# Performance work log

Measured on AMD Instinct MI355X. Metric: run time of the kernel, lower is better.

Reference implementation:

```python
import jax, jax.numpy as jnp
import numpy as np

B, S, E, H = 2, 2048, 1024, 16
DH = E // H
SCALE = DH ** -0.5


def setup_inputs() -> dict:
    key = jax.random.key(0)
    ks = jax.random.split(key, 11)
    def xavier(k, shape):
        fan_in, fan_out = shape[1], shape[0]
        limit = float(np.sqrt(6.0 / (fan_in + fan_out)))
        return jax.random.uniform(k, shape, jnp.float32, -limit, limit)
    return {
        "q": jax.random.normal(ks[0], (B, S, E), jnp.float32),
        "k": jax.random.normal(ks[1], (B, S, E), jnp.float32),
        "v": jax.random.normal(ks[2], (B, S, E), jnp.float32),
        # torch nn.Linear convention: weight is [out_dim, in_dim]
        "Wq": xavier(ks[3], (E, E)), "bq": jnp.zeros((E,), jnp.float32),
        "Wk": xavier(ks[4], (E, E)), "bk": jnp.zeros((E,), jnp.float32),
        "Wv": xavier(ks[5], (E, E)), "bv": jnp.zeros((E,), jnp.float32),
        "Wo": xavier(ks[6], (E, E)), "bo": jnp.zeros((E,), jnp.float32),
    }


def _to_heads(x):
    # [B, S, E] -> [B, H, S, DH]
    b, s, _ = x.shape
    return x.reshape(b, s, H, DH).transpose(0, 2, 1, 3)


def reference(q, k, v, Wq, bq, Wk, bk, Wv, bv, Wo, bo):
    # projections (activation is identity: activation=None)
    qp = q @ Wq.T + bq
    kp = k @ Wk.T + bk
    vp = v @ Wv.T + bv
    qp = qp * SCALE
    qh, kh, vh = _to_heads(qp), _to_heads(kp), _to_heads(vp)
    # full attention scores, materialized as in the original bmm path
    raw = jnp.einsum("bhqd,bhkd->bhqk", qh, kh)  # [B, H, S, S]
    weights = jax.nn.softmax(raw, axis=-1)
    out = jnp.einsum("bhqk,bhkd->bhqd", weights, vh)  # [B, H, S, DH]
    out = out.transpose(0, 2, 1, 3).reshape(B, S, E)
    out = out @ Wo.T + bo
    return out, weights
```

## Files before the change

### kernel.cpp

```cpp
#include <hip/hip_runtime.h>

typedef unsigned short u16;
typedef short bf16x8 __attribute__((ext_vector_type(8)));
typedef float f32x4 __attribute__((ext_vector_type(4)));


__device__ __forceinline__ u16 f2bf(float f) {
    union { float f; unsigned u; } v; v.f = f;
    unsigned r = v.u + 0x7fffu + ((v.u >> 16) & 1u);
    return (u16)(r >> 16);
}
__device__ __forceinline__ unsigned pk2(float a, float b) {
    return (unsigned)f2bf(a) | ((unsigned)f2bf(b) << 16);
}
__device__ __forceinline__ uint4 pk8(const float4& x, const float4& y) {
    uint4 r; r.x = pk2(x.x, x.y); r.y = pk2(x.z, x.w);
    r.z = pk2(y.x, y.y); r.w = pk2(y.z, y.w); return r;
}

template <int MODE>
__global__ __launch_bounds__(256) void gemm_nt(
    const float* __restrict__ A, const float* __restrict__ W,
    const float* __restrict__ bias, u16* __restrict__ out, float scale)
{
    __shared__ u16 As[128 * 32];
    __shared__ u16 Bs[128 * 32];
    const int t = threadIdx.x;
    const int lane = t & 63, wid = t >> 6;
    const int wm = wid >> 1, wn = wid & 1;
    const int qd = lane >> 4, c = lane & 15;
    const int mbase = blockIdx.y * 128, nbase = blockIdx.x * 128;

    f32x4 acc[4][4] = {};

    const int rr = t >> 2, cc = (t & 3) * 8;
    for (int k0 = 0; k0 < 1024; k0 += 32) {
#pragma unroll
        for (int it = 0; it < 2; ++it) {
            int r = rr + it * 64;
            const float* pa = &A[(size_t)(mbase + r) * 1024 + k0 + cc];
            const float* pw = &W[(size_t)(nbase + r) * 1024 + k0 + cc];
            *(uint4*)&As[r * 32 + cc] =
                pk8(*(const float4*)pa, *(const float4*)(pa + 4));
            *(uint4*)&Bs[r * 32 + cc] =
                pk8(*(const float4*)pw, *(const float4*)(pw + 4));
        }
        __syncthreads();
        bf16x8 af[4], bfr[4];
#pragma unroll
        for (int i = 0; i < 4; ++i)
            af[i] = *(const bf16x8*)&As[(wm * 64 + i * 16 + c) * 32 + qd * 8];
#pragma unroll
        for (int j = 0; j < 4; ++j)
            bfr[j] = *(const bf16x8*)&Bs[(wn * 64 + j * 16 + c) * 32 + qd * 8];
#pragma unroll
        for (int i = 0; i < 4; ++i)
#pragma unroll
            for (int j = 0; j < 4; ++j)
                acc[i][j] = __builtin_amdgcn_mfma_f32_16x16x32_bf16(
                    af[i], bfr[j], acc[i][j], 0, 0, 0);
        __syncthreads();
    }

#pragma unroll
    for (int j = 0; j < 4; ++j) {
        const int n = nbase + wn * 64 + j * 16 + c;
        const float bv = bias[n];
#pragma unroll
        for (int i = 0; i < 4; ++i) {
#pragma unroll
            for (int r = 0; r < 4; ++r) {
                const int m = mbase + wm * 64 + i * 16 + qd * 4 + r;
                const float val = (acc[i][j][r] + bv) * scale;
                int b = m >> 11, s = m & 2047, h = n >> 6, d = n & 63;
                size_t dst;
                if (MODE == 0)
                    dst = ((size_t)(b * 16 + h) * 2048 + s) * 64 + d;
                else
                    dst = ((size_t)(b * 16 + h) * 64 + d) * 2048 + s;
                out[dst] = f2bf(val);
            }
        }
    }
}

__global__ __launch_bounds__(256) void gemm_out(
    const u16* __restrict__ A, const float* __restrict__ W,
    const float* __restrict__ bias, float* __restrict__ out)
{
    __shared__ u16 As[128 * 32];
    __shared__ u16 Bs[128 * 32];
    const int t = threadIdx.x;
    const int lane = t & 63, wid = t >> 6;
    const int wm = wid >> 1, wn = wid & 1;
    const int qd = lane >> 4, c = lane & 15;
    const int mbase = blockIdx.y * 128, nbase = blockIdx.x * 128;

    f32x4 acc[4][4] = {};

    const int rr = t >> 2, cc = (t & 3) * 8;
    for (int k0 = 0; k0 < 1024; k0 += 32) {
#pragma unroll
        for (int it = 0; it < 2; ++it) {
            int r = rr + it * 64;
            *(uint4*)&As[r * 32 + cc] =
                *(const uint4*)&A[(size_t)(mbase + r) * 1024 + k0 + cc];
            const float* pw = &W[(size_t)(nbase + r) * 1024 + k0 + cc];
            *(uint4*)&Bs[r * 32 + cc] =
                pk8(*(const float4*)pw, *(const float4*)(pw + 4));
        }
        __syncthreads();
        bf16x8 af[4], bfr[4];
#pragma unroll
        for (int i = 0; i < 4; ++i)
            af[i] = *(const bf16x8*)&As[(wm * 64 + i * 16 + c) * 32 + qd * 8];
#pragma unroll
        for (int j = 0; j < 4; ++j)
            bfr[j] = *(const bf16x8*)&Bs[(wn * 64 + j * 16 + c) * 32 + qd * 8];
#pragma unroll
        for (int i = 0; i < 4; ++i)
#pragma unroll
            for (int j = 0; j < 4; ++j)
                acc[i][j] = __builtin_amdgcn_mfma_f32_16x16x32_bf16(
                    af[i], bfr[j], acc[i][j], 0, 0, 0);
        __syncthreads();
    }

#pragma unroll
    for (int j = 0; j < 4; ++j) {
        const int n = nbase + wn * 64 + j * 16 + c;
        const float bv = bias[n];
#pragma unroll
        for (int i = 0; i < 4; ++i)
#pragma unroll
            for (int r = 0; r < 4; ++r) {
                const int m = mbase + wm * 64 + i * 16 + qd * 4 + r;
                out[(size_t)m * 1024 + n] = acc[i][j][r] + bv;
            }
    }
}

__global__ __launch_bounds__(256) void attn_weights(
    const u16* __restrict__ Qp, const u16* __restrict__ Kp,
    float* __restrict__ Wout)
{
    __shared__ u16 Qs[128 * 64];
    __shared__ u16 Ks[128 * 64];
    __shared__ float lsum[128];
    const int t = threadIdx.x;
    const int lane = t & 63, wid = t >> 6;
    const int wm = wid >> 1, wn = wid & 1;
    const int qd = lane >> 4, c = lane & 15;
    const int bh = blockIdx.y;
    const int qbase = blockIdx.x * 128;
    const u16* Qb = Qp + (size_t)bh * 2048 * 64 + (size_t)qbase * 64;
    const u16* Kb = Kp + (size_t)bh * 2048 * 64;
    float* Wb = Wout + (size_t)bh * 2048 * 2048;

#pragma unroll
    for (int it = 0; it < 4; ++it)
        ((uint4*)Qs)[it * 256 + t] = ((const uint4*)Qb)[it * 256 + t];
    if (t < 128) lsum[t] = 0.f;
    __syncthreads();

    for (int kt = 0; kt < 16; ++kt) {
#pragma unroll
        for (int it = 0; it < 4; ++it)
            ((uint4*)Ks)[it * 256 + t] =
                ((const uint4*)(Kb + (size_t)kt * 128 * 64))[it * 256 + t];
        __syncthreads();
        f32x4 acc[4][4] = {};
#pragma unroll
        for (int ks = 0; ks < 2; ++ks) {
            bf16x8 af[4], bfr[4];
#pragma unroll
            for (int i = 0; i < 4; ++i)
                af[i] = *(const bf16x8*)&Qs[(wm * 64 + i * 16 + c) * 64 + ks * 32 + qd * 8];
#pragma unroll
            for (int j = 0; j < 4; ++j)
                bfr[j] = *(const bf16x8*)&Ks[(wn * 64 + j * 16 + c) * 64 + ks * 32 + qd * 8];
#pragma unroll
            for (int i = 0; i < 4; ++i)
#pragma unroll
                for (int j = 0; j < 4; ++j)
                    acc[i][j] = __builtin_amdgcn_mfma_f32_16x16x32_bf16(
                        af[i], bfr[j], acc[i][j], 0, 0, 0);
        }
#pragma unroll
        for (int i = 0; i < 4; ++i) {
#pragma unroll
            for (int r = 0; r < 4; ++r) {
                float s = 0.f;
#pragma unroll
                for (int j = 0; j < 4; ++j) s += __expf(acc[i][j][r]);
                s += __shfl_xor(s, 1);
                s += __shfl_xor(s, 2);
                s += __shfl_xor(s, 4);
                s += __shfl_xor(s, 8);
                if (c == 0) atomicAdd(&lsum[wm * 64 + i * 16 + qd * 4 + r], s);
            }
        }
        __syncthreads();
    }

    for (int kt = 0; kt < 16; ++kt) {
#pragma unroll
        for (int it = 0; it < 4; ++it)
            ((uint4*)Ks)[it * 256 + t] =
                ((const uint4*)(Kb + (size_t)kt * 128 * 64))[it * 256 + t];
        __syncthreads();
        f32x4 acc[4][4] = {};
#pragma unroll
        for (int ks = 0; ks < 2; ++ks) {
            bf16x8 af[4], bfr[4];
#pragma unroll
            for (int i = 0; i < 4; ++i)
                af[i] = *(const bf16x8*)&Qs[(wm * 64 + i * 16 + c) * 64 + ks * 32 + qd * 8];
#pragma unroll
            for (int j = 0; j < 4; ++j)
                bfr[j] = *(const bf16x8*)&Ks[(wn * 64 + j * 16 + c) * 64 + ks * 32 + qd * 8];
#pragma unroll
            for (int i = 0; i < 4; ++i)
#pragma unroll
                for (int j = 0; j < 4; ++j)
                    acc[i][j] = __builtin_amdgcn_mfma_f32_16x16x32_bf16(
                        af[i], bfr[j], acc[i][j], 0, 0, 0);
        }
#pragma unroll
        for (int i = 0; i < 4; ++i) {
#pragma unroll
            for (int r = 0; r < 4; ++r) {
                const int row = wm * 64 + i * 16 + qd * 4 + r;
                const float inv = 1.f / lsum[row];
#pragma unroll
                for (int j = 0; j < 4; ++j) {
                    const int col = kt * 128 + wn * 64 + j * 16 + c;
                    Wb[(size_t)(qbase + row) * 2048 + col] =
                        __expf(acc[i][j][r]) * inv;
                }
            }
        }
        __syncthreads();
    }
}

__global__ __launch_bounds__(256) void attn_pv(
    const float* __restrict__ Wout, const u16* __restrict__ Vt,
    u16* __restrict__ AO)
{
    __shared__ u16 Ps[128 * 32];
    __shared__ u16 Vs[64 * 32];
    const int t = threadIdx.x;
    const int lane = t & 63, wid = t >> 6;
    const int qd = lane >> 4, c = lane & 15;
    const int bh = blockIdx.y;
    const int b = bh >> 4, h = bh & 15;
    const int qbase = blockIdx.x * 128;
    const float* Wb = Wout + (size_t)bh * 2048 * 2048 + (size_t)qbase * 2048;
    const u16* Vb = Vt + (size_t)bh * 64 * 2048;

    f32x4 acc[2][4] = {};
    const int rr = t >> 2, cc = (t & 3) * 8;
    for (int j0 = 0; j0 < 2048; j0 += 32) {
#pragma unroll
        for (int it = 0; it < 2; ++it) {
            int r = rr + it * 64;
            const float* pp = &Wb[(size_t)r * 2048 + j0 + cc];
            *(uint4*)&Ps[r * 32 + cc] =
                pk8(*(const float4*)pp, *(const float4*)(pp + 4));
        }
        *(uint4*)&Vs[rr * 32 + cc] =
            *(const uint4*)&Vb[(size_t)rr * 2048 + j0 + cc];
        __syncthreads();
        bf16x8 af[2], bfr[4];
#pragma unroll
        for (int i = 0; i < 2; ++i)
            af[i] = *(const bf16x8*)&Ps[(wid * 32 + i * 16 + c) * 32 + qd * 8];
#pragma unroll
        for (int j = 0; j < 4; ++j)
            bfr[j] = *(const bf16x8*)&Vs[(j * 16 + c) * 32 + qd * 8];
#pragma unroll
        for (int i = 0; i < 2; ++i)
#pragma unroll
            for (int j = 0; j < 4; ++j)
                acc[i][j] = __builtin_amdgcn_mfma_f32_16x16x32_bf16(
                    af[i], bfr[j], acc[i][j], 0, 0, 0);
        __syncthreads();
    }

#pragma unroll
    for (int i = 0; i < 2; ++i) {
#pragma unroll
        for (int r = 0; r < 4; ++r) {
            const int row = wid * 32 + i * 16 + qd * 4 + r;
#pragma unroll
            for (int j = 0; j < 4; ++j) {
                const int d = j * 16 + c;
                AO[((size_t)b * 2048 + qbase + row) * 1024 + h * 64 + d] =
                    f2bf(acc[i][j][r]);
            }
        }
    }
}

extern "C" void kernel_launch(void* const* d_in, const int* in_sizes, int n_in,
                              void* d_out, int out_size, void* d_ws, size_t ws_size,
                              hipStream_t stream) {
    const float* q  = (const float*)d_in[0];
    const float* k  = (const float*)d_in[1];
    const float* v  = (const float*)d_in[2];
    const float* Wq = (const float*)d_in[3];
    const float* bq = (const float*)d_in[4];
    const float* Wk = (const float*)d_in[5];
    const float* bk = (const float*)d_in[6];
    const float* Wv = (const float*)d_in[7];
    const float* bv = (const float*)d_in[8];
    const float* Wo = (const float*)d_in[9];
    const float* bo = (const float*)d_in[10];

    float* out  = (float*)d_out;
    float* wout = out + (size_t)4194304;

    u16* Qp = (u16*)d_ws;
    u16* Kp = Qp + (size_t)4194304;
    u16* Vt = Kp + (size_t)4194304;
    u16* AO = Qp;

    dim3 blk(256);
    gemm_nt<0><<<dim3(8, 32), blk, 0, stream>>>(q, Wq, bq, Qp, 0.125f);
    gemm_nt<0><<<dim3(8, 32), blk, 0, stream>>>(k, Wk, bk, Kp, 1.0f);
    gemm_nt<1><<<dim3(8, 32), blk, 0, stream>>>(v, Wv, bv, Vt, 1.0f);
    attn_weights<<<dim3(16, 32), blk, 0, stream>>>(Qp, Kp, wout);
    attn_pv<<<dim3(16, 32), blk, 0, stream>>>(wout, Vt, AO);
    gemm_out<<<dim3(8, 32), blk, 0, stream>>>(AO, Wo, bo, out);
}
```

Measured before the change: 1.078 ms.

## Fuse attention weights and PV into one kernel with swizzled shared memory

Merges the softmax-weights kernel and the PV matmul kernel so the normalized probabilities are written to global memory once and also kept as bf16 in shared memory, where they feed the PV MFMAs directly. This avoids re-reading the 512MB-scale fp32 weight tensor from HBM. It also adds XOR swizzling of the Q/K/P shared tiles to reduce bank conflicts, remaps block indices for locality, and writes attention output in head-major layout, which the output GEMM reads through modified indexing. In exchange it uses more shared memory and reads V directly from global memory without staging.

```diff
diff --git a/kernel.cpp b/kernel.cpp
--- a/kernel.cpp
+++ b/kernel.cpp
@@ -103,9 +103,12 @@
 #pragma unroll
         for (int it = 0; it < 2; ++it) {
             int r = rr + it * 64;
-            *(uint4*)&As[r * 32 + cc] =
-                *(const uint4*)&A[(size_t)(mbase + r) * 1024 + k0 + cc];
-            const float* pw = &W[(size_t)(nbase + r) * 1024 + k0 + cc];
+            const int m = mbase + r;
+            const int b = m >> 11, s = m & 2047;
+            const int kk = k0 + cc;
+            *(uint4*)&As[r * 32 + cc] = *(const uint4*)&A[
+                ((size_t)(b * 16 + (kk >> 6)) * 2048 + s) * 64 + (kk & 63)];
+            const float* pw = &W[(size_t)(nbase + r) * 1024 + kk];
             *(uint4*)&Bs[r * 32 + cc] =
                 pk8(*(const float4*)pw, *(const float4*)(pw + 4));
         }
@@ -140,45 +143,65 @@
     }
 }
 
-__global__ __launch_bounds__(256) void attn_weights(
-    const u16* __restrict__ Qp, const u16* __restrict__ Kp,
+__global__ __launch_bounds__(256, 2) void attn_fused(
+    u16* QAO ,
+    const u16* __restrict__ Kp, const u16* __restrict__ Vt,
     float* __restrict__ Wout)
 {
     __shared__ u16 Qs[128 * 64];
     __shared__ u16 Ks[128 * 64];
-    __shared__ float lsum[128];
+    __shared__ u16 Ps[128 * 128];
+    float* lsum = (float*)Ps;
+
     const int t = threadIdx.x;
     const int lane = t & 63, wid = t >> 6;
     const int wm = wid >> 1, wn = wid & 1;
     const int qd = lane >> 4, c = lane & 15;
-    const int bh = blockIdx.y;
-    const int qbase = blockIdx.x * 128;
-    const u16* Qb = Qp + (size_t)bh * 2048 * 64 + (size_t)qbase * 64;
+
+    const int hw = blockIdx.y * gridDim.x + blockIdx.x;
+    const int L = (hw & 7) * 64 + (hw >> 3);
+    const int bh = L >> 4;
+    const int qbase = (L & 15) * 128;
+
+    const u16* Qb = QAO + (size_t)bh * 2048 * 64 + (size_t)qbase * 64;
     const u16* Kb = Kp + (size_t)bh * 2048 * 64;
+    const u16* Vb = Vt + (size_t)bh * 64 * 2048;
     float* Wb = Wout + (size_t)bh * 2048 * 2048;
 
 #pragma unroll
-    for (int it = 0; it < 4; ++it)
-        ((uint4*)Qs)[it * 256 + t] = ((const uint4*)Qb)[it * 256 + t];
+    for (int it = 0; it < 4; ++it) {
+        int idx = it * 256 + t;
+        int row = idx >> 3, slot = idx & 7;
+        ((uint4*)Qs)[row * 8 + (slot ^ (row & 7))] = ((const uint4*)Qb)[idx];
+    }
     if (t < 128) lsum[t] = 0.f;
     __syncthreads();
 
     for (int kt = 0; kt < 16; ++kt) {
-#pragma unroll
-        for (int it = 0; it < 4; ++it)
-            ((uint4*)Ks)[it * 256 + t] =
-                ((const uint4*)(Kb + (size_t)kt * 128 * 64))[it * 256 + t];
+        const uint4* src = (const uint4*)(Kb + (size_t)kt * 128 * 64);
+#pragma unroll
+        for (int it = 0; it < 4; ++it) {
+            int idx = it * 256 + t;
+            int row = idx >> 3, slot = idx & 7;
+            ((uint4*)Ks)[row * 8 + (slot ^ (row & 7))] = src[idx];
+        }
         __syncthreads();
         f32x4 acc[4][4] = {};
 #pragma unroll
         for (int ks = 0; ks < 2; ++ks) {
             bf16x8 af[4], bfr[4];
 #pragma unroll
-            for (int i = 0; i < 4; ++i)
-                af[i] = *(const bf16x8*)&Qs[(wm * 64 + i * 16 + c) * 64 + ks * 32 + qd * 8];
-#pragma unroll
-            for (int j = 0; j < 4; ++j)
-                bfr[j] = *(const bf16x8*)&Ks[(wn * 64 + j * 16 + c) * 64 + ks * 32 + qd * 8];
+            for (int i = 0; i < 4; ++i) {
+                const int row = wm * 64 + i * 16 + c;
+                af[i] = *(const bf16x8*)&Qs[row * 64 +
+                        (((ks * 4 + qd) ^ (row & 7)) << 3)];
+            }
+#pragma unroll
+            for (int j = 0; j < 4; ++j) {
+                const int row = wn * 64 + j * 16 + c;
+                bfr[j] = *(const bf16x8*)&Ks[row * 64 +
+                        (((ks * 4 + qd) ^ (row & 7)) << 3)];
+            }
 #pragma unroll
             for (int i = 0; i < 4; ++i)
 #pragma unroll
@@ -203,22 +226,41 @@
         __syncthreads();
     }
 
+    float inv[4][4];
+#pragma unroll
+    for (int i = 0; i < 4; ++i)
+#pragma unroll
+        for (int r = 0; r < 4; ++r)
+            inv[i][r] = 1.f / lsum[wm * 64 + i * 16 + qd * 4 + r];
+    __syncthreads();
+
+    f32x4 accv[2][4] = {};
+
     for (int kt = 0; kt < 16; ++kt) {
-#pragma unroll
-        for (int it = 0; it < 4; ++it)
-            ((uint4*)Ks)[it * 256 + t] =
-                ((const uint4*)(Kb + (size_t)kt * 128 * 64))[it * 256 + t];
+        const uint4* src = (const uint4*)(Kb + (size_t)kt * 128 * 64);
+#pragma unroll
+        for (int it = 0; it < 4; ++it) {
+            int idx = it * 256 + t;
+            int row = idx >> 3, slot = idx & 7;
+            ((uint4*)Ks)[row * 8 + (slot ^ (row & 7))] = src[idx];
+        }
         __syncthreads();
         f32x4 acc[4][4] = {};
 #pragma unroll
         for (int ks = 0; ks < 2; ++ks) {
             bf16x8 af[4], bfr[4];
 #pragma unroll
-            for (int i = 0; i < 4; ++i)
-                af[i] = *(const bf16x8*)&Qs[(wm * 64 + i * 16 + c) * 64 + ks * 32 + qd * 8];
-#pragma unroll
-            for (int j = 0; j < 4; ++j)
-                bfr[j] = *(const bf16x8*)&Ks[(wn * 64 + j * 16 + c) * 64 + ks * 32 + qd * 8];
+            for (int i = 0; i < 4; ++i) {
+                const int row = wm * 64 + i * 16 + c;
+                af[i] = *(const bf16x8*)&Qs[row * 64 +
+                        (((ks * 4 + qd) ^ (row & 7)) << 3)];
+            }
+#pragma unroll
+            for (int j = 0; j < 4; ++j) {
+                const int row = wn * 64 + j * 16 + c;
+                bfr[j] = *(const bf16x8*)&Ks[row * 64 +
+                        (((ks * 4 + qd) ^ (row & 7)) << 3)];
+            }
 #pragma unroll
             for (int i = 0; i < 4; ++i)
 #pragma unroll
@@ -231,74 +273,49 @@
 #pragma unroll
             for (int r = 0; r < 4; ++r) {
                 const int row = wm * 64 + i * 16 + qd * 4 + r;
-                const float inv = 1.f / lsum[row];
 #pragma unroll
                 for (int j = 0; j < 4; ++j) {
-                    const int col = kt * 128 + wn * 64 + j * 16 + c;
-                    Wb[(size_t)(qbase + row) * 2048 + col] =
-                        __expf(acc[i][j][r]) * inv;
+                    const int lcol = wn * 64 + j * 16 + c;
+                    const float w = __expf(acc[i][j][r]) * inv[i][r];
+                    Wb[(size_t)(qbase + row) * 2048 + kt * 128 + lcol] = w;
+                    const int slot = lcol >> 3;
+                    Ps[row * 128 + ((slot ^ (row & 15)) << 3) + (c & 7)] =
+                        f2bf(w);
                 }
             }
         }
         __syncthreads();
-    }
-}
-
-__global__ __launch_bounds__(256) void attn_pv(
-    const float* __restrict__ Wout, const u16* __restrict__ Vt,
-    u16* __restrict__ AO)
-{
-    __shared__ u16 Ps[128 * 32];
-    __shared__ u16 Vs[64 * 32];
-    const int t = threadIdx.x;
-    const int lane = t & 63, wid = t >> 6;
-    const int qd = lane >> 4, c = lane & 15;
-    const int bh = blockIdx.y;
-    const int b = bh >> 4, h = bh & 15;
-    const int qbase = blockIdx.x * 128;
-    const float* Wb = Wout + (size_t)bh * 2048 * 2048 + (size_t)qbase * 2048;
-    const u16* Vb = Vt + (size_t)bh * 64 * 2048;
-
-    f32x4 acc[2][4] = {};
-    const int rr = t >> 2, cc = (t & 3) * 8;
-    for (int j0 = 0; j0 < 2048; j0 += 32) {
-#pragma unroll
-        for (int it = 0; it < 2; ++it) {
-            int r = rr + it * 64;
-            const float* pp = &Wb[(size_t)r * 2048 + j0 + cc];
-            *(uint4*)&Ps[r * 32 + cc] =
-                pk8(*(const float4*)pp, *(const float4*)(pp + 4));
-        }
-        *(uint4*)&Vs[rr * 32 + cc] =
-            *(const uint4*)&Vb[(size_t)rr * 2048 + j0 + cc];
-        __syncthreads();
-        bf16x8 af[2], bfr[4];
-#pragma unroll
-        for (int i = 0; i < 2; ++i)
-            af[i] = *(const bf16x8*)&Ps[(wid * 32 + i * 16 + c) * 32 + qd * 8];
-#pragma unroll
-        for (int j = 0; j < 4; ++j)
-            bfr[j] = *(const bf16x8*)&Vs[(j * 16 + c) * 32 + qd * 8];
-#pragma unroll
-        for (int i = 0; i < 2; ++i)
-#pragma unroll
-            for (int j = 0; j < 4; ++j)
-                acc[i][j] = __builtin_amdgcn_mfma_f32_16x16x32_bf16(
-                    af[i], bfr[j], acc[i][j], 0, 0, 0);
-        __syncthreads();
-    }
-
-#pragma unroll
-    for (int i = 0; i < 2; ++i) {
+#pragma unroll
+        for (int ks2 = 0; ks2 < 4; ++ks2) {
+            bf16x8 pa[2], vbr[4];
+#pragma unroll
+            for (int i2 = 0; i2 < 2; ++i2) {
+                const int row = wid * 32 + i2 * 16 + c;
+                pa[i2] = *(const bf16x8*)&Ps[row * 128 +
+                        (((ks2 * 4 + qd) ^ (row & 15)) << 3)];
+            }
+#pragma unroll
+            for (int jj = 0; jj < 4; ++jj)
+                vbr[jj] = *(const bf16x8*)&Vb[(size_t)(jj * 16 + c) * 2048 +
+                        kt * 128 + ks2 * 32 + qd * 8];
+#pragma unroll
+            for (int i2 = 0; i2 < 2; ++i2)
+#pragma unroll
+                for (int jj = 0; jj < 4; ++jj)
+                    accv[i2][jj] = __builtin_amdgcn_mfma_f32_16x16x32_bf16(
+                        pa[i2], vbr[jj], accv[i2][jj], 0, 0, 0);
+        }
+    }
+
+    u16* AOb = QAO + (size_t)bh * 2048 * 64 + (size_t)qbase * 64;
+#pragma unroll
+    for (int i2 = 0; i2 < 2; ++i2) {
 #pragma unroll
         for (int r = 0; r < 4; ++r) {
-            const int row = wid * 32 + i * 16 + qd * 4 + r;
-#pragma unroll
-            for (int j = 0; j < 4; ++j) {
-                const int d = j * 16 + c;
-                AO[((size_t)b * 2048 + qbase + row) * 1024 + h * 64 + d] =
-                    f2bf(acc[i][j][r]);
-            }
+            const int row = wid * 32 + i2 * 16 + qd * 4 + r;
+#pragma unroll
+            for (int jj = 0; jj < 4; ++jj)
+                AOb[(size_t)row * 64 + jj * 16 + c] = f2bf(accv[i2][jj][r]);
         }
     }
 }
@@ -324,13 +341,11 @@
     u16* Qp = (u16*)d_ws;
     u16* Kp = Qp + (size_t)4194304;
     u16* Vt = Kp + (size_t)4194304;
-    u16* AO = Qp;
 
     dim3 blk(256);
     gemm_nt<0><<<dim3(8, 32), blk, 0, stream>>>(q, Wq, bq, Qp, 0.125f);
     gemm_nt<0><<<dim3(8, 32), blk, 0, stream>>>(k, Wk, bk, Kp, 1.0f);
     gemm_nt<1><<<dim3(8, 32), blk, 0, stream>>>(v, Wv, bv, Vt, 1.0f);
-    attn_weights<<<dim3(16, 32), blk, 0, stream>>>(Qp, Kp, wout);
-    attn_pv<<<dim3(16, 32), blk, 0, stream>>>(wout, Vt, AO);
-    gemm_out<<<dim3(8, 32), blk, 0, stream>>>(AO, Wo, bo, out);
-}
+    attn_fused<<<dim3(16, 32), blk, 0, stream>>>(Qp, Kp, Vt, wout);
+    gemm_out<<<dim3(8, 32), blk, 0, stream>>>(Qp , Wo, bo, out);
+}
```

Result: faster. 939.4 us (-12.9%).
